# Performance work log

Measured on AMD Instinct MI355X. Metric: run time of the kernel, lower is better.

## Reference

```python
import jax, jax.numpy as jnp
import numpy as np

TK_W = 0.6
G_W = 0.4
HN_W = 0.5
HN_K = 2
EPS_CLIP = 1e-4


def setup_inputs() -> dict:
    key = jax.random.key(0)
    B, C = 4096, 8192
    k1, k2, k3, k4, k5 = jax.random.split(key, 5)
    # probabilities strictly inside (0,1) so BCE logs are finite
    tk_scores = jnp.clip(jax.random.uniform(k1, (B, C), jnp.float32), EPS_CLIP, 1.0 - EPS_CLIP)
    g_scores = jnp.clip(jax.random.uniform(k2, (B, C), jnp.float32), EPS_CLIP, 1.0 - EPS_CLIP)
    # binary 0/1 float targets (sparse positives)
    tk_targets = (jax.random.uniform(k3, (B, C), jnp.float32) > 0.9).astype(jnp.float32)
    g_targets = (jax.random.uniform(k4, (B, C), jnp.float32) > 0.9).astype(jnp.float32)
    confidences = jax.random.uniform(k5, (B,), jnp.float32)
    return {"tk_scores": tk_scores, "g_scores": g_scores,
            "tk_targets": tk_targets, "g_targets": g_targets,
            "confidences": confidences}


def _bce(p, t):
    # BCELoss(reduction='none'): -(t*log(p) + (1-t)*log(1-p))
    return -(t * jnp.log(p) + (1.0 - t) * jnp.log1p(-p))


def _hard_negative_mask(preds, targets, k):
    # top (3k) predictions per row, then first k whose target < 0.5 (in descending-score order)
    B, C = preds.shape
    top_k = max(1, min(C, k * 3))
    _, idx = jax.lax.top_k(preds, top_k)                       # [B, top_k], sorted desc
    tgt_at = jnp.take_along_axis(targets, idx, axis=1) < 0.5   # [B, top_k] is-negative
    cum = jnp.cumsum(tgt_at.astype(jnp.int32), axis=1)
    sel = tgt_at & (cum <= k)                                  # first k negatives only
    rows = jnp.arange(B)[:, None]
    return jnp.zeros_like(preds).at[rows, idx].add(sel.astype(preds.dtype))


def _directional_loss(scores, targets, conf_w):
    loss_mat = _bce(scores, targets)
    pos = (loss_mat * conf_w).mean()
    mask = _hard_negative_mask(jax.lax.stop_gradient(scores), targets, HN_K)
    msum = mask.sum()
    # if mask sum is 0 the numerator is 0 too, so unconditional form matches torch branch
    neg = (loss_mat * mask).sum() / (msum + 1e-8)
    return pos + HN_W * neg


def reference(tk_scores, g_scores, tk_targets, g_targets, confidences):
    conf_w = confidences[:, None]
    tk_loss = _directional_loss(tk_scores, tk_targets, conf_w)
    g_loss = _directional_loss(g_scores, g_targets, conf_w)
    total = TK_W * tk_loss + G_W * g_loss
    return total, tk_loss, g_loss
```

## Files before the change

### kernel.cpp

```cpp
#include <hip/hip_runtime.h>

#define NB 4096
#define NC 8192

__global__ __launch_bounds__(256) void row_stats(
    const float* __restrict__ tk_s, const float* __restrict__ g_s,
    const float* __restrict__ tk_t, const float* __restrict__ g_t,
    const float* __restrict__ conf, float* __restrict__ ws) {
  const int lane = threadIdx.x & 63;
  const int wave = threadIdx.x >> 6;
  const int row  = (blockIdx.x << 2) + wave;
  const int mat  = blockIdx.y;

  const float4* S4 = reinterpret_cast<const float4*>(
      (mat ? g_s : tk_s) + (size_t)row * NC);
  const float4* T4 = reinterpret_cast<const float4*>(
      (mat ? g_t : tk_t) + (size_t)row * NC);

  unsigned lk0=0,lk1=0,lk2=0,lk3=0,lk4=0,lk5=0;
  unsigned lp0=0,lp1=0,lp2=0,lp3=0,lp4=0,lp5=0;
  float bsum = 0.0f;
  unsigned tseed;

  float4 s = S4[lane];
  float4 t = T4[lane];
  {
    float m4 = fmaxf(fmaxf(s.x, s.y), fmaxf(s.z, s.w));
    m4 = fmaxf(m4, __shfl_xor(m4, 1));
    m4 = fmaxf(m4, __shfl_xor(m4, 2));
    m4 = fmaxf(m4, __shfl_xor(m4, 4));
    m4 = fminf(m4, __shfl_xor(m4, 8));
    m4 = fminf(m4, __shfl_xor(m4, 16));
    m4 = fminf(m4, __shfl_xor(m4, 32));
    tseed = __float_as_uint(m4) - 1u;
  }

#define INS(KJ, PJ) { if (ck_ > KJ) { unsigned tk_ = KJ, tp_ = PJ;        \
    KJ = ck_; PJ = cp_; ck_ = tk_; cp_ = tp_; } }

  auto process = [&](float4 sv, float4 tv, int i) {
#define ELEM(se, te, e) {                                                 \
    float p_ = (se);                                                      \
    bool pos_ = (te) > 0.5f;                                              \
    float arg_ = pos_ ? p_ : (1.0f - p_);                                 \
    bsum += __logf(arg_);                                                 \
    unsigned kb_ = __float_as_uint(p_);                                   \
    unsigned thr_ = lk5 > tseed ? lk5 : tseed;                            \
    unsigned long long m_ = __ballot(kb_ > thr_);                         \
    if (m_) {                                                             \
      unsigned long long pm_ = __ballot(pos_);                            \
      do {                                                                \
        int l_ = __ffsll(m_) - 1;                                         \
        m_ &= m_ - 1;                                                     \
        unsigned key_ = __builtin_amdgcn_readlane(kb_, l_);               \
        if (key_ > lk5) {                                                 \
          unsigned ck_ = key_;                                            \
          unsigned cp_ = ((unsigned)(((i) * 64 + l_) * 4 + (e)) << 1) |   \
                         (unsigned)((pm_ >> l_) & 1ull);                  \
          INS(lk0, lp0) INS(lk1, lp1) INS(lk2, lp2)                       \
          INS(lk3, lp3) INS(lk4, lp4) INS(lk5, lp5)                       \
        }                                                                 \
      } while (m_);                                                       \
    }                                                                     \
  }
    ELEM(sv.x, tv.x, 0)
    ELEM(sv.y, tv.y, 1)
    ELEM(sv.z, tv.z, 2)
    ELEM(sv.w, tv.w, 3)
#undef ELEM
  };

  for (int i = 0; i < 31; ++i) {
    float4 sn = S4[(i + 1) * 64 + lane];
    float4 tn = T4[(i + 1) * 64 + lane];
    process(s, t, i);
    s = sn; t = tn;
  }
  process(s, t, 31);
#undef INS

  #pragma unroll
  for (int off = 32; off > 0; off >>= 1) bsum += __shfl_xor(bsum, off);

  if (lane == 0) {
    float nsum = 0.0f; int cnt = 0;
#define SELN(ki, pi) { if (((pi) & 1u) == 0u && cnt < 2) {                \
      nsum += -__logf(1.0f - __uint_as_float(ki)); cnt++; } }
    SELN(lk0, lp0) SELN(lk1, lp1) SELN(lk2, lp2)
    SELN(lk3, lp3) SELN(lk4, lp4) SELN(lk5, lp5)
#undef SELN
    const int base = mat * NB + row;
    ws[base]          = conf[row] * (-bsum);
    ws[2 * NB + base] = nsum;
    ws[4 * NB + base] = (float)cnt;
  }
}

__global__ __launch_bounds__(256) void finalize_loss(
    const float* __restrict__ ws, float* __restrict__ out) {
  __shared__ float red[6][256];
  const int t = threadIdx.x;
  float a[6] = {0.f, 0.f, 0.f, 0.f, 0.f, 0.f};
  for (int r = t; r < NB; r += 256) {
    #pragma unroll
    for (int j = 0; j < 6; ++j) a[j] += ws[j * NB + r];
  }
  #pragma unroll
  for (int j = 0; j < 6; ++j) red[j][t] = a[j];
  __syncthreads();
  for (int s = 128; s > 0; s >>= 1) {
    if (t < s) {
      #pragma unroll
      for (int j = 0; j < 6; ++j) red[j][t] += red[j][t + s];
    }
    __syncthreads();
  }
  if (t == 0) {
    const float inv = 1.0f / ((float)NB * (float)NC);
    float tk = red[0][0] * inv + 0.5f * (red[2][0] / (red[4][0] + 1e-8f));
    float g  = red[1][0] * inv + 0.5f * (red[3][0] / (red[5][0] + 1e-8f));
    out[0] = 0.6f * tk + 0.4f * g;
    out[1] = tk;
    out[2] = g;
  }
}

extern "C" void kernel_launch(void* const* d_in, const int* in_sizes, int n_in,
                              void* d_out, int out_size, void* d_ws, size_t ws_size,
                              hipStream_t stream) {
  const float* tk_s = (const float*)d_in[0];
  const float* g_s  = (const float*)d_in[1];
  const float* tk_t = (const float*)d_in[2];
  const float* g_t  = (const float*)d_in[3];
  const float* conf = (const float*)d_in[4];
  float* ws  = (float*)d_ws;
  float* out = (float*)d_out;

  dim3 grid(NB / 4, 2);
  row_stats<<<grid, 256, 0, stream>>>(tk_s, g_s, tk_t, g_t, conf, ws);
  finalize_loss<<<1, 256, 0, stream>>>(ws, out);
}
```

Before: 109.4 us.

## Fuse BCE logs into one log2 per float4 and batch top-k ballots

The per-element BCE log is replaced by a single log2 of the product of |s+t-1| over four elements, using the fact that targets are exactly 0 or 1. This cuts transcendental calls by a factor of four. The top-k candidate test now does one ballot per float4, using the max of its four lanes, instead of one ballot per element. The prefetch pipeline is also deepened to two loads ahead with a 2x unroll. Risks: the product of four probabilities can underflow near 1e-4^4 while staying inside float range, and the abs trick assumes binary targets.

```diff
diff --git a/kernel.cpp b/kernel.cpp
--- a/kernel.cpp
+++ b/kernel.cpp
@@ -19,13 +19,13 @@
 
   unsigned lk0=0,lk1=0,lk2=0,lk3=0,lk4=0,lk5=0;
   unsigned lp0=0,lp1=0,lp2=0,lp3=0,lp4=0,lp5=0;
-  float bsum = 0.0f;
+  float bl2 = 0.0f;
   unsigned tseed;
 
-  float4 s = S4[lane];
-  float4 t = T4[lane];
+  float4 s0 = S4[lane],      t0 = T4[lane];
+  float4 s1 = S4[64 + lane], t1 = T4[64 + lane];
   {
-    float m4 = fmaxf(fmaxf(s.x, s.y), fmaxf(s.z, s.w));
+    float m4 = fmaxf(fmaxf(s0.x, s0.y), fmaxf(s0.z, s0.w));
     m4 = fmaxf(m4, __shfl_xor(m4, 1));
     m4 = fmaxf(m4, __shfl_xor(m4, 2));
     m4 = fmaxf(m4, __shfl_xor(m4, 4));
@@ -37,50 +37,58 @@
 
 #define INS(KJ, PJ) { if (ck_ > KJ) { unsigned tk_ = KJ, tp_ = PJ;        \
     KJ = ck_; PJ = cp_; ck_ = tk_; cp_ = tp_; } }
+#define TRY(KE, QE, CE) { unsigned key_ = __builtin_amdgcn_readlane(KE, l_); \
+    if (key_ > lk5) {                                                     \
+      unsigned ck_ = key_;                                                \
+      unsigned cp_ = ((unsigned)(CE) << 1) |                              \
+                     (unsigned)((QE >> l_) & 1ull);                       \
+      INS(lk0, lp0) INS(lk1, lp1) INS(lk2, lp2)                           \
+      INS(lk3, lp3) INS(lk4, lp4) INS(lk5, lp5)                           \
+    } }
 
   auto process = [&](float4 sv, float4 tv, int i) {
-#define ELEM(se, te, e) {                                                 \
-    float p_ = (se);                                                      \
-    bool pos_ = (te) > 0.5f;                                              \
-    float arg_ = pos_ ? p_ : (1.0f - p_);                                 \
-    bsum += __logf(arg_);                                                 \
-    unsigned kb_ = __float_as_uint(p_);                                   \
-    unsigned thr_ = lk5 > tseed ? lk5 : tseed;                            \
-    unsigned long long m_ = __ballot(kb_ > thr_);                         \
-    if (m_) {                                                             \
-      unsigned long long pm_ = __ballot(pos_);                            \
-      do {                                                                \
-        int l_ = __ffsll(m_) - 1;                                         \
-        m_ &= m_ - 1;                                                     \
-        unsigned key_ = __builtin_amdgcn_readlane(kb_, l_);               \
-        if (key_ > lk5) {                                                 \
-          unsigned ck_ = key_;                                            \
-          unsigned cp_ = ((unsigned)(((i) * 64 + l_) * 4 + (e)) << 1) |   \
-                         (unsigned)((pm_ >> l_) & 1ull);                  \
-          INS(lk0, lp0) INS(lk1, lp1) INS(lk2, lp2)                       \
-          INS(lk3, lp3) INS(lk4, lp4) INS(lk5, lp5)                       \
-        }                                                                 \
-      } while (m_);                                                       \
-    }                                                                     \
-  }
-    ELEM(sv.x, tv.x, 0)
-    ELEM(sv.y, tv.y, 1)
-    ELEM(sv.z, tv.z, 2)
-    ELEM(sv.w, tv.w, 3)
-#undef ELEM
+    float b0 = (sv.x + tv.x) - 1.0f;
+    float b1 = (sv.y + tv.y) - 1.0f;
+    float b2 = (sv.z + tv.z) - 1.0f;
+    float b3 = (sv.w + tv.w) - 1.0f;
+    float pr = (fabsf(b0) * fabsf(b1)) * (fabsf(b2) * fabsf(b3));
+    bl2 += __log2f(pr);
+    float m4 = fmaxf(fmaxf(sv.x, sv.y), fmaxf(sv.z, sv.w));
+    float thrf = __uint_as_float(lk5 > tseed ? lk5 : tseed);
+    unsigned long long m_ = __ballot(m4 > thrf);
+    if (m_) {
+      unsigned long long q0 = __ballot(tv.x > 0.5f);
+      unsigned long long q1 = __ballot(tv.y > 0.5f);
+      unsigned long long q2 = __ballot(tv.z > 0.5f);
+      unsigned long long q3 = __ballot(tv.w > 0.5f);
+      unsigned kx = __float_as_uint(sv.x), ky = __float_as_uint(sv.y);
+      unsigned kz = __float_as_uint(sv.z), kw = __float_as_uint(sv.w);
+      do {
+        int l_ = __ffsll(m_) - 1;
+        m_ &= m_ - 1;
+        unsigned c_ = (unsigned)(((i) * 64 + l_) * 4);
+        TRY(kx, q0, c_)
+        TRY(ky, q1, c_ + 1)
+        TRY(kz, q2, c_ + 2)
+        TRY(kw, q3, c_ + 3)
+      } while (m_);
+    }
   };
 
-  for (int i = 0; i < 31; ++i) {
-    float4 sn = S4[(i + 1) * 64 + lane];
-    float4 tn = T4[(i + 1) * 64 + lane];
-    process(s, t, i);
-    s = sn; t = tn;
+  #pragma unroll 2
+  for (int i = 0; i < 30; ++i) {
+    float4 sn = S4[(i + 2) * 64 + lane];
+    float4 tn = T4[(i + 2) * 64 + lane];
+    process(s0, t0, i);
+    s0 = s1; t0 = t1; s1 = sn; t1 = tn;
   }
-  process(s, t, 31);
+  process(s0, t0, 30);
+  process(s1, t1, 31);
+#undef TRY
 #undef INS
 
   #pragma unroll
-  for (int off = 32; off > 0; off >>= 1) bsum += __shfl_xor(bsum, off);
+  for (int off = 32; off > 0; off >>= 1) bl2 += __shfl_xor(bl2, off);
 
   if (lane == 0) {
     float nsum = 0.0f; int cnt = 0;
@@ -90,7 +98,8 @@
     SELN(lk3, lp3) SELN(lk4, lp4) SELN(lk5, lp5)
 #undef SELN
     const int base = mat * NB + row;
-    ws[base]          = conf[row] * (-bsum);
+    const float ln2 = 0.6931471805599453f;
+    ws[base]          = conf[row] * (-bl2 * ln2);
     ws[2 * NB + base] = nsum;
     ws[4 * NB + base] = (float)cnt;
   }
```

Measured after the change: 109.7 us. About the same (+0.3%).
